# Kernel tuning notes

Measured on AMD Instinct MI355X. Metric: run time of the kernel, lower is better.

## Reference

```python
import jax, jax.numpy as jnp
import numpy as np

B = 262144
D = 16          # input_dim
D2 = D // 2     # 8, == hidden_dim
H = 8           # hidden_dim
L = 15          # num_layers (couplings)
NH = 3          # hidden_block_layers
EPS = 1e-6
SLOPE = 0.01    # LeakyReLU default


def setup_inputs() -> dict:
    key = jax.random.key(0)
    ks = jax.random.split(key, 8)
    z = jax.random.normal(ks[0], (B, D), dtype=jnp.float32)
    s = 0.2  # keep log_s away from the +/-5 clamp saturation
    W_in = jax.random.normal(ks[1], (L, 2, D2, H), dtype=jnp.float32) * s
    b_in = jax.random.normal(ks[2], (L, 2, H), dtype=jnp.float32) * s
    W_hid = jax.random.normal(ks[3], (L, 2, NH, H, H), dtype=jnp.float32) * s
    b_hid = jax.random.normal(ks[4], (L, 2, NH, H), dtype=jnp.float32) * s
    W_out = jax.random.normal(ks[5], (L, 2, H, D2), dtype=jnp.float32) * s
    b_out = jax.random.normal(ks[6], (L, 2, D2), dtype=jnp.float32) * s
    # 14 random permutations between couplings + identity after the last coupling
    rng = np.random.default_rng(0)
    perms = np.stack([rng.permutation(D) for _ in range(L - 1)] + [np.arange(D)])
    perms = jnp.asarray(perms, dtype=jnp.int32)  # [L, D]
    return {"z": z, "W_in": W_in, "b_in": b_in, "W_hid": W_hid,
            "b_hid": b_hid, "W_out": W_out, "b_out": b_out, "perms": perms}


def _mlp(x, Wi, bi, Wh, bh, Wo, bo):
    # LinearBlock: (Linear+LeakyReLU) + NH x (Linear+LeakyReLU) + Linear
    h = jax.nn.leaky_relu(x @ Wi + bi, SLOPE)
    for j in range(NH):  # NH is a small static constant
        h = jax.nn.leaky_relu(h @ Wh[j] + bh[j], SLOPE)
    return h @ Wo + bo


def _flow(z, W_in, b_in, W_hid, b_hid, W_out, b_out, perms):
    def step(carry, params):
        z, ld = carry
        Wi, bi, Wh, bh, Wo, bo, perm = params
        z_l, z_r = z[:, :D2], z[:, D2:]
        log_s = jnp.clip(_mlp(z_l, Wi[0], bi[0], Wh[0], bh[0], Wo[0], bo[0]), -5.0, 5.0)
        b = _mlp(z_l, Wi[1], bi[1], Wh[1], bh[1], Wo[1], bo[1])
        y_r = (jnp.exp(log_s) + EPS) * z_r + b
        y = jnp.concatenate([z_l, y_r], axis=1)
        ld = ld + jnp.sum(log_s, axis=1)
        y = y[:, perm]  # Permutation layer (identity for the last step)
        return (y, ld), None

    ld0 = jnp.zeros(z.shape[0], dtype=z.dtype)
    (y, ld), _ = jax.lax.scan(step, (z, ld0), (W_in, b_in, W_hid, b_hid, W_out, b_out, perms))
    return y, ld


def reference(z, W_in, b_in, W_hid, b_hid, W_out, b_out, perms):
    return _flow(z, W_in, b_in, W_hid, b_hid, W_out, b_out, perms)
```

## Files before the change

### kernel.cpp

```cpp
#include <hip/hip_runtime.h>

#define BN 262144
#define HALF (BN / 2)
#define LNUM 15
#define NSTG 151
#define NF4 (NSTG * 18)

extern "C" __global__ void build_slab(
    const float* __restrict__ Wi, const float* __restrict__ bi,
    const float* __restrict__ Wh, const float* __restrict__ bh,
    const float* __restrict__ Wo, const float* __restrict__ bo,
    float* __restrict__ slab) {
    int idx = blockIdx.x * 256 + threadIdx.x;
    if (idx >= NSTG * 72) return;
    int sl = idx / 72, k = idx % 72;
    if (sl == NSTG - 1) sl = 0;
    const int l = sl / 10, r = sl % 10, net = r / 5, st = r % 5;
    const int nb = l * 2 + net;
    float v;
    if (k < 64) {
        if (st == 0)      v = Wi[nb * 64 + k];
        else if (st < 4)  v = Wh[(nb * 3 + (st - 1)) * 64 + k];
        else              v = Wo[nb * 64 + k];
    } else {
        const int o = k - 64;
        if (st == 0)      v = bi[nb * 8 + o];
        else if (st < 4)  v = bh[(nb * 3 + (st - 1)) * 8 + o];
        else              v = bo[nb * 8 + o];
    }
    slab[idx] = v;
}

#define WB(buf, k) ((k) % 4 == 0 ? buf[(k) / 4].x : (k) % 4 == 1 ? buf[(k) / 4].y \
                  : (k) % 4 == 2 ? buf[(k) / 4].z : buf[(k) / 4].w)

#define PREFL(dst, sidx)                                                     \
    {                                                                        \
        const float4* sp = &wls[(sidx) * 18];                                \
        _Pragma("unroll") for (int j = 0; j < 18; ++j) dst[j] = sp[j];       \
    }

__device__ __forceinline__ void mv8x2(const float a[8], const float b[8],
                                      const float4 buf[18],
                                      float oa[8], float ob[8]) {
#pragma unroll
    for (int o = 0; o < 8; ++o) {
        const float w0 = WB(buf, o), bb = WB(buf, 64 + o);
        oa[o] = fmaf(a[0], w0, bb);
        ob[o] = fmaf(b[0], w0, bb);
    }
#pragma unroll
    for (int i = 1; i < 8; ++i)
#pragma unroll
        for (int o = 0; o < 8; ++o) {
            const float w = WB(buf, i * 8 + o);
            oa[o] = fmaf(a[i], w, oa[o]);
            ob[o] = fmaf(b[i], w, ob[o]);
        }
}

__device__ __forceinline__ void lr8(float v[8]) {
#pragma unroll
    for (int o = 0; o < 8; ++o) v[o] = fmaxf(v[o], 0.01f * v[o]);
}

extern "C" __global__ void __launch_bounds__(512, 2) flow_fwd(
    const float* __restrict__ z, const float* __restrict__ slab,
    const int* __restrict__ perms,
    float* __restrict__ outy, float* __restrict__ outld) {
    __shared__ float4 wls[NF4];
    __shared__ float xs[512 * 35];
    const int t = threadIdx.x;
    const long i = (long)blockIdx.x * 512 + t;
    float* __restrict__ mA = &xs[t * 35];
    float* __restrict__ mB = mA + 17;

    {
        const float4* gs = reinterpret_cast<const float4*>(slab);
        for (int k = t; k < NF4; k += 512) wls[k] = gs[k];
    }

    float xA[16], xB[16];
    {
        const float4* zp = reinterpret_cast<const float4*>(z + i * 16);
#pragma unroll
        for (int q = 0; q < 4; ++q) {
            float4 a = zp[q];
            xA[4 * q] = a.x; xA[4 * q + 1] = a.y; xA[4 * q + 2] = a.z; xA[4 * q + 3] = a.w;
        }
        const float4* zq = reinterpret_cast<const float4*>(z + (i + HALF) * 16);
#pragma unroll
        for (int q = 0; q < 4; ++q) {
            float4 a = zq[q];
            xB[4 * q] = a.x; xB[4 * q + 1] = a.y; xB[4 * q + 2] = a.z; xB[4 * q + 3] = a.w;
        }
    }
    float ldA = 0.f, ldB = 0.f;
    __syncthreads();

    float4 A[18], Bq[18];
    PREFL(A, 0)

#pragma unroll 1
    for (int l = 0; l < LNUM; ++l) {
        const int base = l * 10;
        float hA[8], hB[8], gA[8], gB[8], sA[8], sB[8], bA[8], bB[8];
        PREFL(Bq, base + 1)  mv8x2(xA, xB, A,  hA, hB); lr8(hA); lr8(hB);
        PREFL(A,  base + 2)  mv8x2(hA, hB, Bq, gA, gB); lr8(gA); lr8(gB);
        PREFL(Bq, base + 3)  mv8x2(gA, gB, A,  hA, hB); lr8(hA); lr8(hB);
        PREFL(A,  base + 4)  mv8x2(hA, hB, Bq, gA, gB); lr8(gA); lr8(gB);
        PREFL(Bq, base + 5)  mv8x2(gA, gB, A,  sA, sB);
        PREFL(A,  base + 6)  mv8x2(xA, xB, Bq, hA, hB); lr8(hA); lr8(hB);
        PREFL(Bq, base + 7)  mv8x2(hA, hB, A,  gA, gB); lr8(gA); lr8(gB);
        PREFL(A,  base + 8)  mv8x2(gA, gB, Bq, hA, hB); lr8(hA); lr8(hB);
        PREFL(Bq, base + 9)  mv8x2(hA, hB, A,  gA, gB); lr8(gA); lr8(gB);
        PREFL(A,  base + 10) mv8x2(gA, gB, Bq, bA, bB);

#pragma unroll
        for (int k = 0; k < 8; ++k) {
            const float cA = fminf(fmaxf(sA[k], -5.f), 5.f);
            const float cB = fminf(fmaxf(sB[k], -5.f), 5.f);
            ldA += cA; ldB += cB;
            xA[8 + k] = fmaf(__expf(cA) + 1e-6f, xA[8 + k], bA[k]);
            xB[8 + k] = fmaf(__expf(cB) + 1e-6f, xB[8 + k], bB[k]);
        }
#pragma unroll
        for (int p = 0; p < 16; ++p) { mA[p] = xA[p]; mB[p] = xB[p]; }
        const int* __restrict__ pl = perms + l * 16;
#pragma unroll
        for (int j = 0; j < 16; ++j) { xA[j] = mA[pl[j]]; xB[j] = mB[pl[j]]; }
    }

    {
        float4* ya = reinterpret_cast<float4*>(outy + i * 16);
#pragma unroll
        for (int q = 0; q < 4; ++q) {
            float4 a;
            a.x = xA[4 * q]; a.y = xA[4 * q + 1]; a.z = xA[4 * q + 2]; a.w = xA[4 * q + 3];
            ya[q] = a;
        }
        float4* yb = reinterpret_cast<float4*>(outy + (i + HALF) * 16);
#pragma unroll
        for (int q = 0; q < 4; ++q) {
            float4 a;
            a.x = xB[4 * q]; a.y = xB[4 * q + 1]; a.z = xB[4 * q + 2]; a.w = xB[4 * q + 3];
            yb[q] = a;
        }
    }
    outld[i] = ldA;
    outld[i + HALF] = ldB;
}

extern "C" void kernel_launch(void* const* d_in, const int* in_sizes, int n_in,
                              void* d_out, int out_size, void* d_ws, size_t ws_size,
                              hipStream_t stream) {
    const float* z = (const float*)d_in[0];
    const float* Wi = (const float*)d_in[1];
    const float* bi = (const float*)d_in[2];
    const float* Wh = (const float*)d_in[3];
    const float* bh = (const float*)d_in[4];
    const float* Wo = (const float*)d_in[5];
    const float* bo = (const float*)d_in[6];
    const int* perms = (const int*)d_in[7];
    float* out = (float*)d_out;
    float* slab = (float*)d_ws;

    hipLaunchKernelGGL(build_slab, dim3((NSTG * 72 + 255) / 256), dim3(256), 0, stream,
                       Wi, bi, Wh, bh, Wo, bo, slab);
    hipLaunchKernelGGL(flow_fwd, dim3(HALF / 512), dim3(512), 0, stream,
                       z, slab, perms, out, out + (size_t)BN * 16);
}
```

Before: 99.26 us.

## Process four samples per thread to amortize LDS weight reads

Each thread now carries four batch rows instead of two, so every weight value read from shared memory feeds four FMAs instead of two. The block shrinks to 256 threads, the grid to a quarter of the batch, and the permutation scratch grows to 69 floats per thread. The aim is to cut LDS traffic per FLOP. The cost is much higher register pressure: the launch bounds drop to one block per CU with fewer waves, and spills are possible.

```diff
diff --git a/kernel.cpp b/kernel.cpp
--- a/kernel.cpp
+++ b/kernel.cpp
@@ -1,7 +1,8 @@
 #include <hip/hip_runtime.h>
 
 #define BN 262144
-#define HALF (BN / 2)
+#define S4 4
+#define QS (BN / S4)
 #define LNUM 15
 #define NSTG 151
 #define NF4 (NSTG * 18)
@@ -40,62 +41,58 @@
         _Pragma("unroll") for (int j = 0; j < 18; ++j) dst[j] = sp[j];       \
     }
 
-__device__ __forceinline__ void mv8x2(const float a[8], const float b[8],
-                                      const float4 buf[18],
-                                      float oa[8], float ob[8]) {
+template <int LD>
+__device__ __forceinline__ void mv8x4(const float* __restrict__ in,
+                                      const float4 buf[18], float out[4][8]) {
 #pragma unroll
     for (int o = 0; o < 8; ++o) {
         const float w0 = WB(buf, o), bb = WB(buf, 64 + o);
-        oa[o] = fmaf(a[0], w0, bb);
-        ob[o] = fmaf(b[0], w0, bb);
+#pragma unroll
+        for (int s = 0; s < 4; ++s) out[s][o] = fmaf(in[s * LD], w0, bb);
     }
 #pragma unroll
     for (int i = 1; i < 8; ++i)
 #pragma unroll
         for (int o = 0; o < 8; ++o) {
             const float w = WB(buf, i * 8 + o);
-            oa[o] = fmaf(a[i], w, oa[o]);
-            ob[o] = fmaf(b[i], w, ob[o]);
+#pragma unroll
+            for (int s = 0; s < 4; ++s) out[s][o] = fmaf(in[s * LD + i], w, out[s][o]);
         }
 }
 
-__device__ __forceinline__ void lr8(float v[8]) {
+__device__ __forceinline__ void lr8x4(float v[4][8]) {
 #pragma unroll
-    for (int o = 0; o < 8; ++o) v[o] = fmaxf(v[o], 0.01f * v[o]);
+    for (int s = 0; s < 4; ++s)
+#pragma unroll
+        for (int o = 0; o < 8; ++o) v[s][o] = fmaxf(v[s][o], 0.01f * v[s][o]);
 }
 
-extern "C" __global__ void __launch_bounds__(512, 2) flow_fwd(
+extern "C" __global__ void __launch_bounds__(256, 1) flow_fwd(
     const float* __restrict__ z, const float* __restrict__ slab,
     const int* __restrict__ perms,
     float* __restrict__ outy, float* __restrict__ outld) {
     __shared__ float4 wls[NF4];
-    __shared__ float xs[512 * 35];
+    __shared__ float xs[256 * 69];
     const int t = threadIdx.x;
-    const long i = (long)blockIdx.x * 512 + t;
-    float* __restrict__ mA = &xs[t * 35];
-    float* __restrict__ mB = mA + 17;
+    const int i0 = blockIdx.x * 256 + t;
 
     {
         const float4* gs = reinterpret_cast<const float4*>(slab);
-        for (int k = t; k < NF4; k += 512) wls[k] = gs[k];
+        for (int k = t; k < NF4; k += 256) wls[k] = gs[k];
     }
 
-    float xA[16], xB[16];
-    {
-        const float4* zp = reinterpret_cast<const float4*>(z + i * 16);
+    float x[4][16];
+#pragma unroll
+    for (int s = 0; s < 4; ++s) {
+        const float4* zp = reinterpret_cast<const float4*>(z + (long)(i0 + s * QS) * 16);
 #pragma unroll
         for (int q = 0; q < 4; ++q) {
             float4 a = zp[q];
-            xA[4 * q] = a.x; xA[4 * q + 1] = a.y; xA[4 * q + 2] = a.z; xA[4 * q + 3] = a.w;
-        }
-        const float4* zq = reinterpret_cast<const float4*>(z + (i + HALF) * 16);
-#pragma unroll
-        for (int q = 0; q < 4; ++q) {
-            float4 a = zq[q];
-            xB[4 * q] = a.x; xB[4 * q + 1] = a.y; xB[4 * q + 2] = a.z; xB[4 * q + 3] = a.w;
+            x[s][4 * q] = a.x; x[s][4 * q + 1] = a.y;
+            x[s][4 * q + 2] = a.z; x[s][4 * q + 3] = a.w;
         }
     }
-    float ldA = 0.f, ldB = 0.f;
+    float ld[4] = {0.f, 0.f, 0.f, 0.f};
     __syncthreads();
 
     float4 A[18], Bq[18];
@@ -104,51 +101,52 @@
 #pragma unroll 1
     for (int l = 0; l < LNUM; ++l) {
         const int base = l * 10;
-        float hA[8], hB[8], gA[8], gB[8], sA[8], sB[8], bA[8], bB[8];
-        PREFL(Bq, base + 1)  mv8x2(xA, xB, A,  hA, hB); lr8(hA); lr8(hB);
-        PREFL(A,  base + 2)  mv8x2(hA, hB, Bq, gA, gB); lr8(gA); lr8(gB);
-        PREFL(Bq, base + 3)  mv8x2(gA, gB, A,  hA, hB); lr8(hA); lr8(hB);
-        PREFL(A,  base + 4)  mv8x2(hA, hB, Bq, gA, gB); lr8(gA); lr8(gB);
-        PREFL(Bq, base + 5)  mv8x2(gA, gB, A,  sA, sB);
-        PREFL(A,  base + 6)  mv8x2(xA, xB, Bq, hA, hB); lr8(hA); lr8(hB);
-        PREFL(Bq, base + 7)  mv8x2(hA, hB, A,  gA, gB); lr8(gA); lr8(gB);
-        PREFL(A,  base + 8)  mv8x2(gA, gB, Bq, hA, hB); lr8(hA); lr8(hB);
-        PREFL(Bq, base + 9)  mv8x2(hA, hB, A,  gA, gB); lr8(gA); lr8(gB);
-        PREFL(A,  base + 10) mv8x2(gA, gB, Bq, bA, bB);
+        float h[4][8], g[4][8], sf[4][8], bf[4][8];
+        PREFL(Bq, base + 1)  mv8x4<16>(&x[0][0], A, h);  lr8x4(h);
+        PREFL(A,  base + 2)  mv8x4<8>(&h[0][0], Bq, g);  lr8x4(g);
+        PREFL(Bq, base + 3)  mv8x4<8>(&g[0][0], A, h);   lr8x4(h);
+        PREFL(A,  base + 4)  mv8x4<8>(&h[0][0], Bq, g);  lr8x4(g);
+        PREFL(Bq, base + 5)  mv8x4<8>(&g[0][0], A, sf);
+        PREFL(A,  base + 6)  mv8x4<16>(&x[0][0], Bq, h); lr8x4(h);
+        PREFL(Bq, base + 7)  mv8x4<8>(&h[0][0], A, g);   lr8x4(g);
+        PREFL(A,  base + 8)  mv8x4<8>(&g[0][0], Bq, h);  lr8x4(h);
+        PREFL(Bq, base + 9)  mv8x4<8>(&h[0][0], A, g);   lr8x4(g);
+        PREFL(A,  base + 10) mv8x4<8>(&g[0][0], Bq, bf);
 
 #pragma unroll
-        for (int k = 0; k < 8; ++k) {
-            const float cA = fminf(fmaxf(sA[k], -5.f), 5.f);
-            const float cB = fminf(fmaxf(sB[k], -5.f), 5.f);
-            ldA += cA; ldB += cB;
-            xA[8 + k] = fmaf(__expf(cA) + 1e-6f, xA[8 + k], bA[k]);
-            xB[8 + k] = fmaf(__expf(cB) + 1e-6f, xB[8 + k], bB[k]);
-        }
+        for (int s = 0; s < 4; ++s)
 #pragma unroll
-        for (int p = 0; p < 16; ++p) { mA[p] = xA[p]; mB[p] = xB[p]; }
+            for (int k = 0; k < 8; ++k) {
+                const float cs = fminf(fmaxf(sf[s][k], -5.f), 5.f);
+                ld[s] += cs;
+                x[s][8 + k] = fmaf(__expf(cs) + 1e-6f, x[s][8 + k], bf[s][k]);
+            }
+        float* __restrict__ ms = &xs[t * 69];
+#pragma unroll
+        for (int s = 0; s < 4; ++s)
+#pragma unroll
+            for (int p = 0; p < 16; ++p) ms[s * 17 + p] = x[s][p];
         const int* __restrict__ pl = perms + l * 16;
 #pragma unroll
-        for (int j = 0; j < 16; ++j) { xA[j] = mA[pl[j]]; xB[j] = mB[pl[j]]; }
+        for (int j = 0; j < 16; ++j) {
+            const int pj = pl[j];
+#pragma unroll
+            for (int s = 0; s < 4; ++s) x[s][j] = ms[s * 17 + pj];
+        }
     }
 
-    {
-        float4* ya = reinterpret_cast<float4*>(outy + i * 16);
+#pragma unroll
+    for (int s = 0; s < 4; ++s) {
+        float4* ya = reinterpret_cast<float4*>(outy + (long)(i0 + s * QS) * 16);
 #pragma unroll
         for (int q = 0; q < 4; ++q) {
             float4 a;
-            a.x = xA[4 * q]; a.y = xA[4 * q + 1]; a.z = xA[4 * q + 2]; a.w = xA[4 * q + 3];
+            a.x = x[s][4 * q]; a.y = x[s][4 * q + 1];
+            a.z = x[s][4 * q + 2]; a.w = x[s][4 * q + 3];
             ya[q] = a;
         }
-        float4* yb = reinterpret_cast<float4*>(outy + (i + HALF) * 16);
-#pragma unroll
-        for (int q = 0; q < 4; ++q) {
-            float4 a;
-            a.x = xB[4 * q]; a.y = xB[4 * q + 1]; a.z = xB[4 * q + 2]; a.w = xB[4 * q + 3];
-            yb[q] = a;
-        }
+        outld[i0 + s * QS] = ld[s];
     }
-    outld[i] = ldA;
-    outld[i + HALF] = ldB;
 }
 
 extern "C" void kernel_launch(void* const* d_in, const int* in_sizes, int n_in,
@@ -167,6 +165,6 @@
 
     hipLaunchKernelGGL(build_slab, dim3((NSTG * 72 + 255) / 256), dim3(256), 0, stream,
                        Wi, bi, Wh, bh, Wo, bo, slab);
-    hipLaunchKernelGGL(flow_fwd, dim3(HALF / 512), dim3(512), 0, stream,
+    hipLaunchKernelGGL(flow_fwd, dim3(QS / 256), dim3(256), 0, stream,
                        z, slab, perms, out, out + (size_t)BN * 16);
 }
```

New measurement: 123.6 us. 24.6% more time.
